# Kernel optimization log

Hardware: AMD Instinct MI355X
Metric: run time of the kernel (lower is better)

Reference implementation:

```python
import jax, jax.numpy as jnp
import numpy as np

B, CIN, H, W = 16, 128, 56, 56
COUT, KH, KW = 256, 3, 3
STRIDE = (1, 1)
PAD = ((1, 1), (1, 1))


def setup_inputs() -> dict:
    key = jax.random.key(0)
    k1, k2, k3 = jax.random.split(key, 3)
    x = jax.random.normal(k1, (B, CIN, H, W), dtype=jnp.float32)
    weight = jax.random.normal(k2, (COUT, CIN, KH, KW), dtype=jnp.float32) * 0.05
    bias = jax.random.normal(k3, (COUT,), dtype=jnp.float32)
    return {"x": x, "weight": weight, "bias": bias}


def reference(x, weight, bias):
    # Conv2d with zero padding, stride 1 -- identical math to the torch
    # unfold+expand+multiply+triple-sum path.
    dn = jax.lax.conv_dimension_numbers(x.shape, weight.shape, ("NCHW", "OIHW", "NCHW"))
    out = jax.lax.conv_general_dilated(x, weight, STRIDE, PAD, dimension_numbers=dn)
    out = out + bias[None, :, None, None]

    # Sparsity of the elementwise product patches * weight.
    # count_nonzero(x_patch * w) over all (b,hw,ww,co,ci,kh,kw) factorizes as
    # sum over windows of conv(1[x!=0], 1[w!=0]) -- same count without
    # materializing the [B,Hw,Ww,Co,Ci,kh,kw] tensor the torch code builds.
    co, ci, kh, kw = weight.shape
    hw, ww = out.shape[2], out.shape[3]
    num_elements = x.shape[0] * hw * ww * co * ci * kh * kw
    nz_map = jax.lax.conv_general_dilated(
        (x != 0).astype(jnp.float32),
        (weight != 0).astype(jnp.float32),
        STRIDE, PAD, dimension_numbers=dn)
    num_nonzero = jnp.sum(nz_map)
    layer_sparsity = (jnp.float32(num_elements) - num_nonzero) / jnp.float32(num_elements)
    return out, layer_sparsity
```

## Files before the change

kernel.cpp:

```cpp
#include <hip/hip_runtime.h>
#include <hip/hip_bf16.h>

typedef __attribute__((ext_vector_type(8))) short bf16x8;
typedef __attribute__((ext_vector_type(8))) unsigned short ushort8;
typedef __attribute__((ext_vector_type(4))) unsigned short ushort4v;
typedef __attribute__((ext_vector_type(4))) float f32x4;
typedef __attribute__((ext_vector_type(4))) unsigned int uint4v;

#define CIN_  128
#define BATCH 16
#define SP_   3136
#define CO_   256
#define NTOT  50176

#define XP_BYTES   13778944
#define WT_BYTES   589824
#define WS_NEEDED  14447104

__device__ __forceinline__ unsigned short f2bf(float f) {
    unsigned int u = __float_as_uint(f);
    u = (u + 0x7fffu + ((u >> 16) & 1u)) >> 16;
    return (unsigned short)u;
}

__device__ __forceinline__ void gl_lds16(const unsigned short* g, unsigned short* l) {
    __builtin_amdgcn_global_load_lds(
        (const __attribute__((address_space(1))) unsigned int*)g,
        (__attribute__((address_space(3))) unsigned int*)l, 16, 0, 0);
}

__global__ __launch_bounds__(256) void k_aux(
    const float* __restrict__ x, const float* __restrict__ w,
    unsigned short* __restrict__ Wt, unsigned short* __restrict__ xp,
    float* __restrict__ Wcnt, float* __restrict__ part)
{
    __shared__ float T[64][65];
    __shared__ float red9[4][9];
    const int blk = blockIdx.x;
    const int tid = threadIdx.x;

    if (blk < 288) {
        int base = (blk * 256 + tid) * 4;
        float4 v = *(const float4*)(w + base);
        #pragma unroll
        for (int j = 0; j < 4; ++j) {
            int e = base + j;
            int co = e / 1152;
            int r  = e - co * 1152;
            int ci = r / 9;
            int koff = r - ci * 9;
            Wt[(koff * 256 + co) * 128 + ci] = f2bf(((const float*)&v)[j]);
        }
    } else if (blk < 576) {
        int lane = tid & 63;
        int j = (blk - 288) * 4 + (tid >> 6);
        float c = 0.f;
        for (int co = lane; co < 256; co += 64)
            c += (w[(size_t)co * 1152 + j] != 0.0f) ? 1.f : 0.f;
        #pragma unroll
        for (int s = 32; s > 0; s >>= 1) c += __shfl_down(c, s, 64);
        if (lane == 0) Wcnt[j] = c;
    } else if (blk < 2624) {
        int bc = blk - 576;
        int ci = bc & 127;
        int b  = bc >> 7;
        const float* xpk = x + (size_t)bc * SP_;
        float cnt[9];
        #pragma unroll
        for (int k = 0; k < 9; ++k) cnt[k] = 0.f;
        for (int e = tid; e < SP_; e += 256) {
            float v = xpk[e];
            if (v != 0.f) {
                int h = e / 56, w_ = e - h * 56;
                float r0 = (h <= 54) ? 1.f : 0.f;
                float r2 = (h >= 1) ? 1.f : 0.f;
                float c0 = (w_ <= 54) ? 1.f : 0.f;
                float c2 = (w_ >= 1) ? 1.f : 0.f;
                cnt[0] += r0 * c0; cnt[1] += r0; cnt[2] += r0 * c2;
                cnt[3] += c0;      cnt[4] += 1.f; cnt[5] += c2;
                cnt[6] += r2 * c0; cnt[7] += r2; cnt[8] += r2 * c2;
            }
        }
        #pragma unroll
        for (int k = 0; k < 9; ++k) {
            #pragma unroll
            for (int s = 32; s > 0; s >>= 1) cnt[k] += __shfl_down(cnt[k], s, 64);
        }
        if ((tid & 63) == 0) {
            #pragma unroll
            for (int k = 0; k < 9; ++k) red9[tid >> 6][k] = cnt[k];
        }
        __syncthreads();
        if (tid < 9) {
            float s = red9[0][tid] + red9[1][tid] + red9[2][tid] + red9[3][tid];
            part[(ci * 9 + tid) * 16 + b] = s;
        }
    } else if (blk < 4192) {
        int i = blk - 2624;
        int sp0 = (i % 49) * 64;
        int rest = i / 49;
        int ci0 = (rest & 1) * 64;
        int b = rest >> 1;
        const float* xb = x + ((size_t)(b * 128 + ci0)) * SP_ + sp0;
        #pragma unroll
        for (int r = 0; r < 16; ++r) {
            const int ci_l = (tid >> 6) * 16 + r;
            const int sp_l = tid & 63;
            T[sp_l][ci_l] = xb[(size_t)ci_l * SP_ + sp_l];
        }
        __syncthreads();
        #pragma unroll
        for (int r = 0; r < 4; ++r) {
            const int sp_l = (tid >> 4) * 4 + r;
            const int cc   = (tid & 15) * 4;
            const int sp = sp0 + sp_l;
            const int oh = sp / 56, ow = sp - oh * 56;
            ushort4v v;
            #pragma unroll
            for (int j = 0; j < 4; ++j) v[j] = f2bf(T[sp_l][cc + j]);
            *(ushort4v*)&xp[(((size_t)b * 58 + oh + 1) * 58 + (ow + 1)) * 128 + ci0 + cc] = v;
        }
    } else {
        int b = blk - 4192;
        if (tid < 228) {
            int oh, ow;
            if (tid < 58)       { oh = 0;            ow = tid; }
            else if (tid < 116) { oh = 57;           ow = tid - 58; }
            else if (tid < 172) { oh = tid - 116 + 1; ow = 0; }
            else                { oh = tid - 172 + 1; ow = 57; }
            unsigned short* p = xp + (((size_t)b * 58 + oh) * 58 + ow) * 128;
            ushort8 z = {};
            #pragma unroll
            for (int j = 0; j < 16; ++j) *(ushort8*)(p + j * 8) = z;
        }
    }
}

__global__ void k_spars(const float* __restrict__ Wcnt, const float* __restrict__ part,
                        float* __restrict__ out_scalar) {
    __shared__ double red[256];
    int t = threadIdx.x;
    double s = 0.0;
    for (int j = t; j < 1152; j += 256) {
        const float4* p4 = (const float4*)(part + (size_t)j * 16);
        float4 a = p4[0], b = p4[1], c = p4[2], d = p4[3];
        float xs = (a.x + a.y + a.z + a.w) + (b.x + b.y + b.z + b.w)
                 + (c.x + c.y + c.z + c.w) + (d.x + d.y + d.z + d.w);
        s += (double)Wcnt[j] * (double)xs;
    }
    red[t] = s; __syncthreads();
    for (int k = 128; k > 0; k >>= 1) {
        if (t < k) red[t] += red[t + k];
        __syncthreads();
    }
    if (t == 0) {
        const double ne = 14797504512.0;
        out_scalar[0] = (float)((ne - red[0]) / ne);
    }
}

__global__ __launch_bounds__(256) void k_conv2(
    const unsigned short* __restrict__ xp, const unsigned short* __restrict__ Wt,
    const float* __restrict__ bias, float* __restrict__ out)
{
    __shared__ __attribute__((aligned(16))) unsigned short Alds[2 * 4096];
    __shared__ __attribute__((aligned(16))) unsigned short Blds[2 * 4096];

    const int tid  = threadIdx.x;
    const int lane = tid & 63;
    const int w    = tid >> 6;
    const int wm   = w >> 1, wn = w & 1;

    const int flat = blockIdx.x;
    const int wg   = (flat & 7) * 98 + (flat >> 3);
    const int n0   = (wg >> 1) * 128;
    const int co0  = (wg & 1) * 128;

    int aoff[2], boff[2];
    #pragma unroll
    for (int q = 0; q < 2; ++q) {
        int g   = (w * 2 + q) * 64 + lane;
        int row = g >> 2;
        int c   = (g & 3) ^ ((row >> 1) & 3);
        aoff[q] = (co0 + row) * 128 + c * 8;
        int n  = n0 + row;
        int b  = n / SP_;
        int sp = n - b * SP_;
        int oh = sp / 56, ow = sp - oh * 56;
        boff[q] = ((b * 58 + oh + 1) * 58 + (ow + 1)) * 128 + c * 8;
    }

    f32x4 acc[4][4] = {};
    const int l15 = lane & 15;
    const int pc  = (lane >> 4) ^ ((l15 >> 1) & 3);

    auto stage = [&](int t, int buf) {
        int koff = t >> 2, ksub = t & 3;
        int kd   = koff / 3;
        int dh   = kd - 1, dw = koff - kd * 3 - 1;
        int ash  = koff * 32768 + ksub * 32;
        int bsh  = (dh * 58 + dw) * 128 + ksub * 32;
        #pragma unroll
        for (int q = 0; q < 2; ++q) {
            gl_lds16(Wt + ash + aoff[q], &Alds[buf * 4096 + (w * 2 + q) * 512]);
            gl_lds16(xp + bsh + boff[q], &Blds[buf * 4096 + (w * 2 + q) * 512]);
        }
    };

    stage(0, 0);

    #pragma unroll 2
    for (int t = 0; t < 36; ++t) {
        const int cur = t & 1;
        if (t < 35) {
            stage(t + 1, cur ^ 1);
            asm volatile("s_waitcnt vmcnt(4)" ::: "memory");
        } else {
            asm volatile("s_waitcnt vmcnt(0)" ::: "memory");
        }
        asm volatile("s_barrier" ::: "memory");

        bf16x8 a[4], bb[4];
        #pragma unroll
        for (int m = 0; m < 4; ++m)
            a[m] = *(const bf16x8*)&Alds[cur * 4096 + (wm * 64 + m * 16 + l15) * 32 + pc * 8];
        #pragma unroll
        for (int n = 0; n < 4; ++n)
            bb[n] = *(const bf16x8*)&Blds[cur * 4096 + (wn * 64 + n * 16 + l15) * 32 + pc * 8];
        #pragma unroll
        for (int m = 0; m < 4; ++m)
            #pragma unroll
            for (int n = 0; n < 4; ++n)
                acc[m][n] = __builtin_amdgcn_mfma_f32_16x16x32_bf16(a[m], bb[n], acc[m][n], 0, 0, 0);

        asm volatile("s_barrier" ::: "memory");
    }

    const int rb = (lane >> 4) * 4;
    #pragma unroll
    for (int nf = 0; nf < 4; ++nf) {
        int n  = n0 + wn * 64 + nf * 16 + l15;
        int b  = n / SP_;
        int sp = n - b * SP_;
        float* op = out + (size_t)b * CO_ * SP_ + sp;
        #pragma unroll
        for (int m = 0; m < 4; ++m) {
            int co = co0 + wm * 64 + m * 16 + rb;
            #pragma unroll
            for (int r = 0; r < 4; ++r)
                op[(size_t)(co + r) * SP_] = acc[m][nf][r] + bias[co + r];
        }
    }
}

__global__ void k_wt(const float* __restrict__ w, unsigned short* __restrict__ Wt) {
    int e = blockIdx.x * 256 + threadIdx.x;
    float v = w[e];
    int co = e / 1152;
    int r  = e - co * 1152;
    int ci = r / 9;
    int koff = r - ci * 9;
    Wt[(koff * 256 + co) * 128 + ci] = f2bf(v);
}

__global__ void k_wcnt(const float* __restrict__ w, float* __restrict__ Wcnt) {
    int j = blockIdx.x;
    int lane = threadIdx.x;
    float c = 0.f;
    for (int co = lane; co < 256; co += 64)
        c += (w[(size_t)co * 1152 + j] != 0.0f) ? 1.f : 0.f;
    #pragma unroll
    for (int s = 32; s > 0; s >>= 1) c += __shfl_down(c, s, 64);
    if (lane == 0) Wcnt[j] = c;
}

__global__ void k_xcnt(const float* __restrict__ x, float* __restrict__ Xcnt) {
    int blk = blockIdx.x;
    int ci = blk & 127;
    const float* xpk = x + (size_t)blk * SP_;
    int tid = threadIdx.x;
    float cnt[9];
    #pragma unroll
    for (int k = 0; k < 9; ++k) cnt[k] = 0.f;
    for (int e = tid; e < SP_; e += 256) {
        float v = xpk[e];
        if (v != 0.f) {
            int h = e / 56, w_ = e - h * 56;
            float r0 = (h <= 54) ? 1.f : 0.f;
            float r2 = (h >= 1) ? 1.f : 0.f;
            float c0 = (w_ <= 54) ? 1.f : 0.f;
            float c2 = (w_ >= 1) ? 1.f : 0.f;
            cnt[0] += r0 * c0; cnt[1] += r0; cnt[2] += r0 * c2;
            cnt[3] += c0;      cnt[4] += 1.f; cnt[5] += c2;
            cnt[6] += r2 * c0; cnt[7] += r2; cnt[8] += r2 * c2;
        }
    }
    #pragma unroll
    for (int k = 0; k < 9; ++k) {
        #pragma unroll
        for (int s = 32; s > 0; s >>= 1) cnt[k] += __shfl_down(cnt[k], s, 64);
    }
    if ((tid & 63) == 0) {
        #pragma unroll
        for (int k = 0; k < 9; ++k)
            atomicAdd(&Xcnt[ci * 9 + k], cnt[k]);
    }
}

__global__ void k_spars_f(const float* __restrict__ Wcnt, const float* __restrict__ Xcnt,
                          float* __restrict__ out_scalar) {
    __shared__ double red[256];
    int t = threadIdx.x;
    double s = 0.0;
    for (int j = t; j < 1152; j += 256)
        s += (double)Wcnt[j] * (double)Xcnt[j];
    red[t] = s; __syncthreads();
    for (int k = 128; k > 0; k >>= 1) {
        if (t < k) red[t] += red[t + k];
        __syncthreads();
    }
    if (t == 0) {
        const double ne = 14797504512.0;
        out_scalar[0] = (float)((ne - red[0]) / ne);
    }
}

__global__ __launch_bounds__(256) void k_conv(
    const float* __restrict__ x, const unsigned short* __restrict__ Wt,
    const float* __restrict__ bias, float* __restrict__ out)
{
    __shared__ __attribute__((aligned(16))) unsigned short AldsF[64][40];
    __shared__ __attribute__((aligned(16))) unsigned short BldsF[64][40];

    const int tid  = threadIdx.x;
    const int lane = tid & 63;
    const int wid  = tid >> 6;
    const int wm   = wid >> 1, wn = wid & 1;

    const int n0  = blockIdx.x * 64;
    const int b   = blockIdx.x / 49;
    const int sp0 = n0 - b * SP_;
    const int co0 = blockIdx.y * 64;

    const int a_co = tid >> 2;
    const int a_ci = (tid & 3) * 8;
    const int b_n  = tid & 63;
    const int b_k0 = (tid >> 6) * 8;

    const int sp = sp0 + b_n;
    const int oh = sp / 56, ow = sp - oh * 56;

    f32x4 acc[2][2] = {};
    const float* xb_base = x + (size_t)b * CIN_ * SP_;

    for (int koff = 0; koff < 9; ++koff) {
        const int dh = koff / 3 - 1, dw = koff - (koff / 3) * 3 - 1;
        const int ih = oh + dh, iw = ow + dw;
        const bool valid = ((unsigned)ih < 56u) && ((unsigned)iw < 56u);
        const float* xb = xb_base + sp + dh * 56 + dw;
        const unsigned short* wp = Wt + ((size_t)(koff * 256 + co0 + a_co)) * 128 + a_ci;

        for (int ci0 = 0; ci0 < 128; ci0 += 32) {
            uint4v av = *(const uint4v*)(wp + ci0);
            *(uint4v*)&AldsF[a_co][a_ci] = av;
            ushort8 bv;
            #pragma unroll
            for (int j = 0; j < 8; ++j) {
                int ci = ci0 + b_k0 + j;
                float v = 0.f;
                if (valid) v = xb[(size_t)ci * SP_];
                bv[j] = f2bf(v);
            }
            *(ushort8*)&BldsF[b_n][b_k0] = bv;
            __syncthreads();

            const int row = lane & 15;
            const int kq  = (lane >> 4) * 8;
            bf16x8 a0 = *(const bf16x8*)&AldsF[wm * 32 + row][kq];
            bf16x8 a1 = *(const bf16x8*)&AldsF[wm * 32 + 16 + row][kq];
            bf16x8 bb0 = *(const bf16x8*)&BldsF[wn * 32 + row][kq];
            bf16x8 bb1 = *(const bf16x8*)&BldsF[wn * 32 + 16 + row][kq];
            acc[0][0] = __builtin_amdgcn_mfma_f32_16x16x32_bf16(a0, bb0, acc[0][0], 0, 0, 0);
            acc[0][1] = __builtin_amdgcn_mfma_f32_16x16x32_bf16(a0, bb1, acc[0][1], 0, 0, 0);
            acc[1][0] = __builtin_amdgcn_mfma_f32_16x16x32_bf16(a1, bb0, acc[1][0], 0, 0, 0);
            acc[1][1] = __builtin_amdgcn_mfma_f32_16x16x32_bf16(a1, bb1, acc[1][1], 0, 0, 0);
            __syncthreads();
        }
    }

    const int col = lane & 15;
    const int rb  = (lane >> 4) * 4;
    #pragma unroll
    for (int f = 0; f < 2; ++f) {
        #pragma unroll
        for (int g = 0; g < 2; ++g) {
            int spc = sp0 + wn * 32 + g * 16 + col;
            #pragma unroll
            for (int r = 0; r < 4; ++r) {
                int co = co0 + wm * 32 + f * 16 + rb + r;
                out[((size_t)(b * CO_ + co)) * SP_ + spc] = acc[f][g][r] + bias[co];
            }
        }
    }
}

extern "C" void kernel_launch(void* const* d_in, const int* in_sizes, int n_in,
                              void* d_out, int out_size, void* d_ws, size_t ws_size,
                              hipStream_t stream) {
    const float* x    = (const float*)d_in[0];
    const float* w    = (const float*)d_in[1];
    const float* bias = (const float*)d_in[2];
    float* out = (float*)d_out;

    if (ws_size >= (size_t)WS_NEEDED) {
        unsigned short* xp = (unsigned short*)d_ws;
        unsigned short* Wt = (unsigned short*)((char*)d_ws + XP_BYTES);
        float* Wcnt = (float*)((char*)d_ws + XP_BYTES + WT_BYTES);
        float* part = Wcnt + 1152;

        hipLaunchKernelGGL(k_aux,   dim3(4208),   dim3(256), 0, stream,
                           x, w, Wt, xp, Wcnt, part);
        hipLaunchKernelGGL(k_conv2, dim3(784),    dim3(256), 0, stream, xp, Wt, bias, out);
        hipLaunchKernelGGL(k_spars, dim3(1),      dim3(256), 0, stream, Wcnt, part,
                           out + 12845056);
    } else {
        unsigned short* Wt = (unsigned short*)d_ws;
        float* Wcnt = (float*)((char*)d_ws + WT_BYTES);
        float* Xcnt = Wcnt + 1152;

        hipMemsetAsync((void*)Xcnt, 0, 1152 * sizeof(float), stream);
        hipLaunchKernelGGL(k_wt,      dim3(1152),    dim3(256), 0, stream, w, Wt);
        hipLaunchKernelGGL(k_wcnt,    dim3(1152),    dim3(64),  0, stream, w, Wcnt);
        hipLaunchKernelGGL(k_xcnt,    dim3(2048),    dim3(256), 0, stream, x, Xcnt);
        hipLaunchKernelGGL(k_conv,    dim3(784, 4),  dim3(256), 0, stream, x, Wt, bias, out);
        hipLaunchKernelGGL(k_spars_f, dim3(1),       dim3(256), 0, stream, Wcnt, Xcnt,
                           out + 12845056);
    }
}
```

Measured before the change: 75.28 us.

## Enlarge conv GEMM tile to 256x256 with 8-wave blocks and split-K phases

Replaces the 128x128 four-wave conv kernel with a 256(spatial)x256(all channels) tile per 512-thread block. The loop now runs 18 K-steps of 64 channels, each split into two double-buffered 32-channel phases, with a new LDS swizzle and an MFMA priority boost. Output is written as vectorized 4-wide stores along the spatial dimension. This is meant to raise arithmetic intensity and cut redundant global loads. The trade-off is 196 blocks with large LDS use, which may leave compute units idle.

New measurement: 66.51 us. -11.7%, faster.

```diff
diff --git a/kernel.cpp b/kernel.cpp
--- a/kernel.cpp
+++ b/kernel.cpp
@@ -159,96 +159,116 @@
     }
 }
 
-__global__ __launch_bounds__(256) void k_conv2(
+__global__ __launch_bounds__(512, 2) void k_conv8(
     const unsigned short* __restrict__ xp, const unsigned short* __restrict__ Wt,
     const float* __restrict__ bias, float* __restrict__ out)
 {
-    __shared__ __attribute__((aligned(16))) unsigned short Alds[2 * 4096];
-    __shared__ __attribute__((aligned(16))) unsigned short Blds[2 * 4096];
+    __shared__ __attribute__((aligned(16))) unsigned short Albs[2 * 16384];
+    __shared__ __attribute__((aligned(16))) unsigned short Blbs[2 * 16384];
 
     const int tid  = threadIdx.x;
     const int lane = tid & 63;
+    const int l15  = lane & 15;
     const int w    = tid >> 6;
-    const int wm   = w >> 1, wn = w & 1;
-
-    const int flat = blockIdx.x;
-    const int wg   = (flat & 7) * 98 + (flat >> 3);
-    const int n0   = (wg >> 1) * 128;
-    const int co0  = (wg & 1) * 128;
-
-    int aoff[2], boff[2];
-    #pragma unroll
-    for (int q = 0; q < 2; ++q) {
-        int g   = (w * 2 + q) * 64 + lane;
+    const int wm   = w >> 2;
+    const int wn   = w & 3;
+    const int n0   = blockIdx.x * 256;
+
+    int xoffA[2], woffB[2];
+    #pragma unroll
+    for (int j = 0; j < 2; ++j) {
+        int g   = j * 512 + tid;
         int row = g >> 2;
-        int c   = (g & 3) ^ ((row >> 1) & 3);
-        aoff[q] = (co0 + row) * 128 + c * 8;
-        int n  = n0 + row;
+        int c   = (g & 3) ^ ((row ^ (row >> 2)) & 3);
+        int n   = n0 + row;
+        int b   = n / SP_;
+        int sp  = n - b * SP_;
+        int oh  = sp / 56, ow = sp - oh * 56;
+        xoffA[j] = ((b * 58 + oh + 1) * 58 + (ow + 1)) * 128 + c * 8;
+        woffB[j] = row * 128 + c * 8;
+    }
+
+    auto stageA = [&](int nb, int xsh, int s) {
+        #pragma unroll
+        for (int j = 0; j < 2; ++j)
+            gl_lds16(xp + xsh + s * 32 + xoffA[j],
+                     &Albs[nb + s * 8192 + (j * 512 + tid) * 8]);
+    };
+    auto stageB = [&](int nb, int wsh, int s) {
+        #pragma unroll
+        for (int j = 0; j < 2; ++j)
+            gl_lds16(Wt + wsh + s * 32 + woffB[j],
+                     &Blbs[nb + s * 8192 + (j * 512 + tid) * 8]);
+    };
+
+    f32x4 acc[8][4] = {};
+
+    const int cl = lane >> 4;
+
+#define LDA_(bo, S, R) \
+    (*(const bf16x8*)&Albs[(bo) + (S) * 8192 + ((R) + l15) * 32 + \
+        ((cl ^ ((((R) + l15) ^ (((R) + l15) >> 2)) & 3)) * 8)])
+#define LDB_(bo, S, R) \
+    (*(const bf16x8*)&Blbs[(bo) + (S) * 8192 + ((R) + l15) * 32 + \
+        ((cl ^ ((((R) + l15) ^ (((R) + l15) >> 2)) & 3)) * 8)])
+
+#define PHASE(BO, S, DO_STAGE, NB, XSH, WSH, VMN)                          \
+    {                                                                      \
+        if (DO_STAGE) { stageA(NB, XSH, S); stageB(NB, WSH, S); }          \
+        asm volatile("s_waitcnt vmcnt(" VMN ")" ::: "memory");             \
+        __builtin_amdgcn_s_barrier();                                      \
+        bf16x8 a_[8], b_[4];                                               \
+        _Pragma("unroll")                                                  \
+        for (int m = 0; m < 8; ++m) a_[m] = LDA_(BO, S, wm * 128 + m * 16);\
+        _Pragma("unroll")                                                  \
+        for (int nn = 0; nn < 4; ++nn) b_[nn] = LDB_(BO, S, wn * 64 + nn * 16);\
+        asm volatile("s_waitcnt lgkmcnt(0)" ::: "memory");                 \
+        __builtin_amdgcn_sched_barrier(0);                                 \
+        __builtin_amdgcn_s_setprio(1);                                     \
+        _Pragma("unroll")                                                  \
+        for (int m = 0; m < 8; ++m)                                        \
+            _Pragma("unroll")                                              \
+            for (int nn = 0; nn < 4; ++nn)                                 \
+                acc[m][nn] = __builtin_amdgcn_mfma_f32_16x16x32_bf16(      \
+                    a_[m], b_[nn], acc[m][nn], 0, 0, 0);                   \
+        __builtin_amdgcn_s_setprio(0);                                     \
+    }
+
+    {
+        const int xsh0 = (-59) * 128;
+        const int wsh0 = 0;
+        stageA(0, xsh0, 0); stageB(0, wsh0, 0);
+        stageA(0, xsh0, 1); stageB(0, wsh0, 1);
+    }
+
+    for (int kt = 0; kt < 17; ++kt) {
+        const int bo = (kt & 1) << 14;
+        const int nb = 16384 - bo;
+        const int kn = kt + 1;
+        const int koffn = kn >> 1;
+        const int kdn = koffn / 3;
+        const int xshn = ((kdn - 1) * 58 + (koffn - kdn * 3 - 1)) * 128 + (kn & 1) * 64;
+        const int wshn = koffn * 32768 + (kn & 1) * 64;
+        PHASE(bo, 0, true, nb, xshn, wshn, "8");
+        PHASE(bo, 1, true, nb, xshn, wshn, "8");
+    }
+    PHASE(16384, 0, false, 0, 0, 0, "4");
+    PHASE(16384, 1, false, 0, 0, 0, "0");
+
+#undef PHASE
+#undef LDA_
+#undef LDB_
+
+    #pragma unroll
+    for (int m = 0; m < 8; ++m) {
+        int n  = n0 + wm * 128 + m * 16 + (lane >> 4) * 4;
         int b  = n / SP_;
         int sp = n - b * SP_;
-        int oh = sp / 56, ow = sp - oh * 56;
-        boff[q] = ((b * 58 + oh + 1) * 58 + (ow + 1)) * 128 + c * 8;
-    }
-
-    f32x4 acc[4][4] = {};
-    const int l15 = lane & 15;
-    const int pc  = (lane >> 4) ^ ((l15 >> 1) & 3);
-
-    auto stage = [&](int t, int buf) {
-        int koff = t >> 2, ksub = t & 3;
-        int kd   = koff / 3;
-        int dh   = kd - 1, dw = koff - kd * 3 - 1;
-        int ash  = koff * 32768 + ksub * 32;
-        int bsh  = (dh * 58 + dw) * 128 + ksub * 32;
-        #pragma unroll
-        for (int q = 0; q < 2; ++q) {
-            gl_lds16(Wt + ash + aoff[q], &Alds[buf * 4096 + (w * 2 + q) * 512]);
-            gl_lds16(xp + bsh + boff[q], &Blds[buf * 4096 + (w * 2 + q) * 512]);
-        }
-    };
-
-    stage(0, 0);
-
-    #pragma unroll 2
-    for (int t = 0; t < 36; ++t) {
-        const int cur = t & 1;
-        if (t < 35) {
-            stage(t + 1, cur ^ 1);
-            asm volatile("s_waitcnt vmcnt(4)" ::: "memory");
-        } else {
-            asm volatile("s_waitcnt vmcnt(0)" ::: "memory");
-        }
-        asm volatile("s_barrier" ::: "memory");
-
-        bf16x8 a[4], bb[4];
-        #pragma unroll
-        for (int m = 0; m < 4; ++m)
-            a[m] = *(const bf16x8*)&Alds[cur * 4096 + (wm * 64 + m * 16 + l15) * 32 + pc * 8];
-        #pragma unroll
-        for (int n = 0; n < 4; ++n)
-            bb[n] = *(const bf16x8*)&Blds[cur * 4096 + (wn * 64 + n * 16 + l15) * 32 + pc * 8];
-        #pragma unroll
-        for (int m = 0; m < 4; ++m)
-            #pragma unroll
-            for (int n = 0; n < 4; ++n)
-                acc[m][n] = __builtin_amdgcn_mfma_f32_16x16x32_bf16(a[m], bb[n], acc[m][n], 0, 0, 0);
-
-        asm volatile("s_barrier" ::: "memory");
-    }
-
-    const int rb = (lane >> 4) * 4;
-    #pragma unroll
-    for (int nf = 0; nf < 4; ++nf) {
-        int n  = n0 + wn * 64 + nf * 16 + l15;
-        int b  = n / SP_;
-        int sp = n - b * SP_;
-        float* op = out + (size_t)b * CO_ * SP_ + sp;
-        #pragma unroll
-        for (int m = 0; m < 4; ++m) {
-            int co = co0 + wm * 64 + m * 16 + rb;
-            #pragma unroll
-            for (int r = 0; r < 4; ++r)
-                op[(size_t)(co + r) * SP_] = acc[m][nf][r] + bias[co + r];
+        #pragma unroll
+        for (int nn = 0; nn < 4; ++nn) {
+            int co = wn * 64 + nn * 16 + l15;
+            f32x4 v = acc[m][nn] + bias[co];
+            *(f32x4*)&out[((size_t)(b * CO_ + co)) * SP_ + sp] = v;
         }
     }
 }
@@ -420,7 +440,7 @@
 
         hipLaunchKernelGGL(k_aux,   dim3(4208),   dim3(256), 0, stream,
                            x, w, Wt, xp, Wcnt, part);
-        hipLaunchKernelGGL(k_conv2, dim3(784),    dim3(256), 0, stream, xp, Wt, bias, out);
+        hipLaunchKernelGGL(k_conv8, dim3(196),    dim3(512), 0, stream, xp, Wt, bias, out);
         hipLaunchKernelGGL(k_spars, dim3(1),      dim3(256), 0, stream, Wcnt, part,
                            out + 12845056);
     } else {
```
